# Kernel tuning notes

Hardware: AMD Instinct MI355X
Metric: run time of the kernel (lower is better)

The kernel has to match this reference:

```python
import jax, jax.numpy as jnp
import numpy as np

B, D, C, P = 1024, 768, 150, 64  # batch, in_feats, num_labels, proj2 dim
POS_M, NEG_M = 0.7, 1.4


def setup_inputs() -> dict:
    key = jax.random.key(0)
    ks = jax.random.split(key, 8)
    return {
        "x": jax.random.normal(ks[0], (B, D), jnp.float32),
        "lb": jax.random.randint(ks[1], (B,), 0, C + 1),
        "mem": jax.random.normal(ks[2], (C, D), jnp.float32),
        "fc_w": jax.random.normal(ks[3], (2 * D, 2 * D), jnp.float32) * 0.02,
        "fc_b": jnp.zeros((2 * D,), jnp.float32),
        "p1_w": jax.random.normal(ks[4], (1, 2 * D), jnp.float32) * 0.02,
        "p1_b": jnp.zeros((1,), jnp.float32),
        "p2_w": jax.random.normal(ks[5], (P, 2 * D), jnp.float32) * 0.02,
        "p2_b": jnp.zeros((P,), jnp.float32),
    }


def reference(x, lb, mem, fc_w, fc_b, p1_w, p1_b, p2_w, p2_b):
    d = x.shape[1]
    # cat([a, b], 1) @ fc_w.T == a @ Wx.T + b @ Wm.T  (exact split of the linear)
    Wx, Wm = fc_w[:, :d], fc_w[:, d:]
    xh = x @ Wx.T + fc_b                                # [B, 2D]

    # --- get_logit ---
    seen_h = jax.nn.relu(xh[:, None, :] + mem @ Wm.T)   # [B, C, 2D]
    seen = jnp.einsum('bce,e->bc', seen_h, p1_w[0]) + p1_b[0]   # [B, C]
    uh = jax.nn.relu(xh)                                # cat([x, zeros]) path
    unseen = uh @ p1_w.T + p1_b                         # [B, 1]
    logits = jnp.concatenate([seen, unseen], axis=1)    # [B, C+1]

    # --- masked log-softmax losses (pos_adapte) ---
    labels = jax.nn.one_hot(lb, C + 1, dtype=jnp.float32)
    th = jnp.zeros_like(labels).at[:, -1].set(1.0)
    labels = labels.at[:, -1].set(0.0)
    p_mask = labels + th
    n_mask = 1.0 - labels
    BIG = 1e30
    loss1 = -(jax.nn.log_softmax(logits - (1.0 - p_mask) * BIG, -1) * labels).sum(1)
    loss2 = -(jax.nn.log_softmax(logits - (1.0 - n_mask) * BIG, -1) * th).sum(1)
    loss_cls = (loss1 + loss2).mean()

    # --- metric loss on unseen embedding ---
    u = uh @ p2_w.T + p2_b                              # [B, 64]
    u = u / jnp.maximum(jnp.linalg.norm(u, axis=1, keepdims=True), 1e-12)
    sq_n = (u * u).sum(1)
    sq = sq_n[:, None] + sq_n[None, :] - 2.0 * (u @ u.T)
    err = sq <= 0.0
    dist = jnp.sqrt(jnp.clip(sq, 1e-16, None)) * (~err).astype(u.dtype)
    same = lb[:, None] == lb[None, :]
    eye = jnp.eye(dist.shape[0], dtype=bool)
    pos = (same & ~eye).astype(dist.dtype)
    neg = (~same).astype(dist.dtype)
    pos_l = (jax.nn.relu(dist - POS_M) * pos).sum() / jnp.maximum(pos.sum(), 1.0)
    neg_l = (jax.nn.relu(NEG_M - dist) * neg).sum() / jnp.maximum(neg.sum(), 1.0)

    return loss_cls + pos_l + neg_l
```

## Files before the change

kernel.cpp:

```cpp
#include <hip/hip_runtime.h>
#include <math.h>

#define B_    1024
#define D_    768
#define C_    150
#define P_    64
#define TWOD  1536
#define NCLS  151
#define CPAD  256

#define ECHUNKS 16
#define ECHUNK  96

#define GSTR  72
#define GBUF  (64 * GSTR)
#define NKT   (D_ / 64)
#define USTRU 120
#define USTR  72

#define NBLK  512

#define OFF_MH      0
#define OFF_XH      (OFF_MH + (C_ * TWOD) / 2)
#define OFF_PARTIAL (OFF_XH + (B_ * TWOD) / 2)
#define OFF_UHF     (OFF_PARTIAL + ECHUNKS * B_ * CPAD)
#define OFF_SQN     (OFF_UHF + (B_ * P_) / 2)
#define OFF_CLS     (OFF_SQN + B_)
#define OFF_PAIR    (OFF_CLS + B_)
#define OFF_BAR     (OFF_PAIR + 1024)

typedef __bf16    bfx8   __attribute__((ext_vector_type(8)));
typedef _Float16  fp16x8 __attribute__((ext_vector_type(8)));
typedef _Float16  h2v    __attribute__((ext_vector_type(2)));
typedef float     f32x4  __attribute__((ext_vector_type(4)));

__device__ inline ushort f2bf(float f) {
    union { float f; unsigned u; } c; c.f = f;
    unsigned r = c.u + 0x7fffu + ((c.u >> 16) & 1u);
    return (ushort)(r >> 16);
}
__device__ inline ushort f2h(float f) {
    _Float16 h = (_Float16)f;
    return __builtin_bit_cast(ushort, h);
}
__device__ inline uint4 pack_bf8(float4 a, float4 b) {
    uint4 r;
    r.x = (unsigned)f2bf(a.x) | ((unsigned)f2bf(a.y) << 16);
    r.y = (unsigned)f2bf(a.z) | ((unsigned)f2bf(a.w) << 16);
    r.z = (unsigned)f2bf(b.x) | ((unsigned)f2bf(b.y) << 16);
    r.w = (unsigned)f2bf(b.z) | ((unsigned)f2bf(b.w) << 16);
    return r;
}
__device__ inline uint4 pack_h8(float4 a, float4 b) {
    uint4 r;
    r.x = (unsigned)f2h(a.x) | ((unsigned)f2h(a.y) << 16);
    r.y = (unsigned)f2h(a.z) | ((unsigned)f2h(a.w) << 16);
    r.z = (unsigned)f2h(b.x) | ((unsigned)f2h(b.y) << 16);
    r.w = (unsigned)f2h(b.z) | ((unsigned)f2h(b.w) << 16);
    return r;
}
__device__ inline unsigned addrelu2(unsigned a, unsigned m) {
    h2v s = __builtin_bit_cast(h2v, a) + __builtin_bit_cast(h2v, m);
    h2v z = {(_Float16)0.f, (_Float16)0.f};
    s = __builtin_elementwise_max(s, z);
    return __builtin_bit_cast(unsigned, s);
}
__device__ inline unsigned relu2(unsigned a) {
    h2v s = __builtin_bit_cast(h2v, a);
    h2v z = {(_Float16)0.f, (_Float16)0.f};
    s = __builtin_elementwise_max(s, z);
    return __builtin_bit_cast(unsigned, s);
}
__device__ inline float dot2acc(unsigned a, unsigned b, float c) {
    return __builtin_amdgcn_fdot2(__builtin_bit_cast(h2v, a),
                                  __builtin_bit_cast(h2v, b), c, false);
}

__device__ __forceinline__ void st_wt_u16(ushort* p, unsigned v) {
    asm volatile("global_store_short %0, %1, off sc0 sc1"
                 :: "v"(p), "v"(v) : "memory");
}
__device__ __forceinline__ void st_wt_f32(float* p, float v) {
    asm volatile("global_store_dword %0, %1, off sc0 sc1"
                 :: "v"(p), "v"(v) : "memory");
}
__device__ __forceinline__ void st_wt_f32x4(float* p, f32x4 v) {
    asm volatile("global_store_dwordx4 %0, %1, off sc0 sc1"
                 :: "v"(p), "v"(v) : "memory");
}

__device__ __forceinline__ void grid_barrier(int* bar, int b)
{
    asm volatile("s_waitcnt vmcnt(0)" ::: "memory");
    __syncthreads();
    if (threadIdx.x == 0) {
        int* arr = bar + (b - 1) * 8 * 16;
        int* gen = bar + 576;
        __hip_atomic_fetch_add(&arr[(blockIdx.x & 7) * 16], 1,
                               __ATOMIC_RELAXED, __HIP_MEMORY_SCOPE_AGENT);
        if (blockIdx.x == 0) {
            for (;;) {
                int s = 0;
#pragma unroll
                for (int k = 0; k < 8; ++k)
                    s += __hip_atomic_load(&arr[k * 16], __ATOMIC_RELAXED,
                                           __HIP_MEMORY_SCOPE_AGENT);
                if (s == NBLK) break;
                __builtin_amdgcn_s_sleep(1);
            }
#pragma unroll
            for (int r = 0; r < 32; ++r)
                __hip_atomic_store(&gen[r * 16], b, __ATOMIC_RELAXED,
                                   __HIP_MEMORY_SCOPE_AGENT);
        } else {
            int* myg = &gen[(blockIdx.x & 31) * 16];
            while (__hip_atomic_load(myg, __ATOMIC_RELAXED,
                                     __HIP_MEMORY_SCOPE_AGENT) < b)
                __builtin_amdgcn_s_sleep(4);
        }
        asm volatile("" ::: "memory");
    }
    __syncthreads();
}

__device__ __forceinline__ void phase_gemm(
    int id, char* smemc,
    const float* __restrict__ x, const float* __restrict__ mem,
    const float* __restrict__ fc_w, const float* __restrict__ fc_b,
    ushort* __restrict__ xh, ushort* __restrict__ mh)
{
    if (id >= 456) return;
    ushort* As = (ushort*)smemc;
    ushort* Bs = (ushort*)(smemc + 2 * GBUF * 2);
    const int t = threadIdx.x;

    const float* A; ushort* Out; int M, m0, n0, koff; bool xblk;
    if (id < 384) {
        xblk = true;  A = x;    Out = xh; M = B_;
        m0 = (id & 15) * 64; n0 = (id >> 4) * 64; koff = 0;
    } else {
        int q = id - 384;
        xblk = false; A = mem;  Out = mh; M = C_;
        m0 = (q % 3) * 64; n0 = (q / 3) * 64; koff = D_;
    }

    const int wave = t >> 6, lane = t & 63;
    const int wm = wave * 16;
    const int fm = lane & 15, quad = lane >> 4;

    const int row_a = t >> 2, qa = (t & 3) * 16;
    const int ar = min(m0 + row_a, M - 1);
    const float* Arow = A + (size_t)ar * D_ + qa;
    const float* Brow = fc_w + (size_t)(n0 + row_a) * TWOD + koff + qa;
    const int lw = row_a * GSTR + qa;

    f32x4 acc[4];
#pragma unroll
    for (int j = 0; j < 4; ++j) {
        float bv = xblk ? fc_b[n0 + j * 16 + fm] : 0.f;
        acc[j] = (f32x4){bv, bv, bv, bv};
    }

    float4 pa0 = *(const float4*)(Arow);
    float4 pa1 = *(const float4*)(Arow + 4);
    float4 pa2 = *(const float4*)(Arow + 8);
    float4 pa3 = *(const float4*)(Arow + 12);
    float4 pb0 = *(const float4*)(Brow);
    float4 pb1 = *(const float4*)(Brow + 4);
    float4 pb2 = *(const float4*)(Brow + 8);
    float4 pb3 = *(const float4*)(Brow + 12);

    for (int kt = 0; kt < NKT; ++kt) {
        ushort* Ad = As + (kt & 1) * GBUF;
        ushort* Bd = Bs + (kt & 1) * GBUF;
        *(uint4*)&Ad[lw]     = pack_bf8(pa0, pa1);
        *(uint4*)&Ad[lw + 8] = pack_bf8(pa2, pa3);
        *(uint4*)&Bd[lw]     = pack_bf8(pb0, pb1);
        *(uint4*)&Bd[lw + 8] = pack_bf8(pb2, pb3);
        __syncthreads();
        if (kt + 1 < NKT) {
            const int k1 = (kt + 1) * 64;
            pa0 = *(const float4*)(Arow + k1);
            pa1 = *(const float4*)(Arow + k1 + 4);
            pa2 = *(const float4*)(Arow + k1 + 8);
            pa3 = *(const float4*)(Arow + k1 + 12);
            pb0 = *(const float4*)(Brow + k1);
            pb1 = *(const float4*)(Brow + k1 + 4);
            pb2 = *(const float4*)(Brow + k1 + 8);
            pb3 = *(const float4*)(Brow + k1 + 12);
        }
#pragma unroll
        for (int ks = 0; ks < 2; ++ks) {
            bfx8 af = *(const bfx8*)&Ad[(wm + fm) * GSTR + ks * 32 + quad * 8];
#pragma unroll
            for (int j = 0; j < 4; ++j) {
                bfx8 bf = *(const bfx8*)&Bd[(j * 16 + fm) * GSTR + ks * 32 + quad * 8];
                acc[j] = __builtin_amdgcn_mfma_f32_16x16x32_bf16(
                    af, bf, acc[j], 0, 0, 0);
            }
        }
    }

#pragma unroll
    for (int j = 0; j < 4; ++j)
#pragma unroll
        for (int r = 0; r < 4; ++r) {
            int row = m0 + wm + quad * 4 + r;
            int col = n0 + j * 16 + fm;
            if (row < M)
                st_wt_u16(&Out[(size_t)row * TWOD + col],
                          (unsigned)f2h(acc[j][r]));
        }
}

__device__ __forceinline__ void phase_fused(
    int id, char* smem,
    const ushort* __restrict__ xh, const ushort* __restrict__ mh,
    const float* __restrict__ p1w, const float* __restrict__ p2w,
    float* __restrict__ partial)
{
    const int t  = threadIdx.x;
    const int b0 = (id & 7) * 128;
    const int y  = (id >> 3) & 3;
    const int z  = id >> 5;
    const int e0 = z * ECHUNK;

    if (y == 3) {
        ushort* Au = (ushort*)smem;
        ushort* Wu = (ushort*)(smem + 30720);
        const int wave = t >> 6, lane = t & 63;
        const int fm = lane & 15, quad = lane >> 4;

        {
            const int row = t >> 1, kh = (t & 1) * 48;
            const ushort* src = xh + (size_t)(b0 + row) * TWOD + e0 + kh;
            uint4 v[6];
#pragma unroll
            for (int i = 0; i < 6; ++i) v[i] = *(const uint4*)&src[i * 8];
#pragma unroll
            for (int i = 0; i < 6; ++i) {
                v[i].x = relu2(v[i].x); v[i].y = relu2(v[i].y);
                v[i].z = relu2(v[i].z); v[i].w = relu2(v[i].w);
                *(uint4*)&Au[row * USTRU + kh + i * 8] = v[i];
            }
        }
        {
            const int row = t >> 2, ks = (t & 3) * 24;
            const float* pw = p2w + (size_t)row * TWOD + e0 + ks;
#pragma unroll
            for (int i = 0; i < 3; ++i) {
                float4 lo = *(const float4*)&pw[i * 8];
                float4 hi = *(const float4*)&pw[i * 8 + 4];
                *(uint4*)&Wu[row * USTRU + ks + i * 8] = pack_h8(lo, hi);
            }
        }
        __syncthreads();

        f32x4 uacc[2][4];
#pragma unroll
        for (int i = 0; i < 2; ++i)
#pragma unroll
            for (int j = 0; j < 4; ++j) uacc[i][j] = (f32x4){0.f, 0.f, 0.f, 0.f};
#pragma unroll
        for (int k0 = 0; k0 < ECHUNK; k0 += 32) {
            fp16x8 af[2], bff[4];
#pragma unroll
            for (int i = 0; i < 2; ++i)
                af[i] = *(const fp16x8*)&Au[(wave * 32 + i * 16 + fm) * USTRU + k0 + quad * 8];
#pragma unroll
            for (int j = 0; j < 4; ++j)
                bff[j] = *(const fp16x8*)&Wu[(j * 16 + fm) * USTRU + k0 + quad * 8];
#pragma unroll
            for (int i = 0; i < 2; ++i)
#pragma unroll
                for (int j = 0; j < 4; ++j)
                    uacc[i][j] = __builtin_amdgcn_mfma_f32_16x16x32_f16(
                        af[i], bff[j], uacc[i][j], 0, 0, 0);
        }
#pragma unroll
        for (int i = 0; i < 2; ++i)
#pragma unroll
            for (int j = 0; j < 4; ++j)
#pragma unroll
                for (int r = 0; r < 4; ++r) {
                    int row = b0 + wave * 32 + i * 16 + quad * 4 + r;
                    st_wt_f32(&partial[((size_t)z * B_ + row) * CPAD + 192 + j * 16 + fm],
                              uacc[i][j][r]);
                }
        return;
    }

    unsigned* xT = (unsigned*)smem;
    unsigned* mT = (unsigned*)(smem + 24576);
    unsigned* wT = (unsigned*)(smem + 36864);
    const int c0 = y * 64;
    const int tm = t & 15, tn = t >> 4;

    {
        const int row = t >> 1, ph = (t & 1) * 48;
        const ushort* src = xh + (size_t)(b0 + row) * TWOD + e0 + ph;
        uint4 v[6];
#pragma unroll
        for (int i = 0; i < 6; ++i) v[i] = *(const uint4*)&src[i * 8];
#pragma unroll
        for (int i = 0; i < 6; ++i) {
            const int ep = (t & 1) * 24 + i * 4;
            xT[(ep + 0) * 128 + row] = v[i].x;
            xT[(ep + 1) * 128 + row] = v[i].y;
            xT[(ep + 2) * 128 + row] = v[i].z;
            xT[(ep + 3) * 128 + row] = v[i].w;
        }
    }
    {
        const int col = t & 63, seg = t >> 6;
        const int gc  = c0 + col;
        uint4 v[3];
        if (gc < C_) {
            const ushort* src = mh + (size_t)gc * TWOD + e0 + seg * 24;
#pragma unroll
            for (int i = 0; i < 3; ++i) v[i] = *(const uint4*)&src[i * 8];
        } else {
#pragma unroll
            for (int i = 0; i < 3; ++i) v[i] = make_uint4(0, 0, 0, 0);
        }
#pragma unroll
        for (int i = 0; i < 3; ++i) {
            const int ep = seg * 12 + i * 4;
            mT[(ep + 0) * 64 + col] = v[i].x;
            mT[(ep + 1) * 64 + col] = v[i].y;
            mT[(ep + 2) * 64 + col] = v[i].z;
            mT[(ep + 3) * 64 + col] = v[i].w;
        }
    }
    if (t < 12) {
        float4 lo = *(const float4*)&p1w[e0 + t * 8];
        float4 hi = *(const float4*)&p1w[e0 + t * 8 + 4];
        uint4 v = pack_h8(lo, hi);
        wT[t * 4 + 0] = v.x; wT[t * 4 + 1] = v.y;
        wT[t * 4 + 2] = v.z; wT[t * 4 + 3] = v.w;
    }
    __syncthreads();

    float acc[8][4] = {};
#pragma unroll 4
    for (int ep = 0; ep < 48; ++ep) {
        uint4 a0 = *(const uint4*)&xT[ep * 128 + tm * 8];
        uint4 a1 = *(const uint4*)&xT[ep * 128 + tm * 8 + 4];
        uint4 mj = *(const uint4*)&mT[ep * 64 + tn * 4];
        const unsigned wv = wT[ep];
        const unsigned aa[8] = {a0.x, a0.y, a0.z, a0.w, a1.x, a1.y, a1.z, a1.w};
        const unsigned mm[4] = {mj.x, mj.y, mj.z, mj.w};
#pragma unroll
        for (int i = 0; i < 8; ++i)
#pragma unroll
            for (int j = 0; j < 4; ++j)
                acc[i][j] = dot2acc(addrelu2(aa[i], mm[j]), wv, acc[i][j]);
    }

#pragma unroll
    for (int i = 0; i < 8; ++i) {
        const int gb = b0 + tm * 8 + i;
        f32x4 v = {acc[i][0], acc[i][1], acc[i][2], acc[i][3]};
        st_wt_f32x4(&partial[((size_t)z * B_ + gb) * CPAD + c0 + tn * 4], v);
    }
}

__device__ __forceinline__ void phase_reduce(
    char* smemc,
    const float* __restrict__ partial,
    const float* __restrict__ p1b, const float* __restrict__ p2b,
    const int* __restrict__ lb,
    ushort* __restrict__ uhf, float* __restrict__ sqn,
    float* __restrict__ clsbuf)
{
    float* sval = (float*)smemc;
    const int t = threadIdx.x;
    for (int b = blockIdx.x; b < B_; b += NBLK) {
        float v = 0.f;
#pragma unroll
        for (int z = 0; z < ECHUNKS; ++z)
            v += partial[((size_t)z * B_ + b) * CPAD + t];
        if (t < NCLS)       v += p1b[0];
        else if (t >= 192)  v += p2b[t - 192];

        sval[t] = v;
        __syncthreads();

        if (t < 64) {
            float uv = sval[192 + t];
            float s = uv * uv;
#pragma unroll
            for (int off = 32; off; off >>= 1) s += __shfl_xor(s, off);
            float inv = 1.f / fmaxf(sqrtf(s), 1e-12f);
            st_wt_u16(&uhf[(size_t)b * P_ + t], (unsigned)f2h(uv * inv));
            if (t == 0) st_wt_f32(&sqn[b], s * inv * inv);

            const int l = lb[b];
            float mx = -1e30f;
            for (int j = t; j < NCLS; j += 64)
                if (!(j == l && l < C_)) mx = fmaxf(mx, sval[j]);
#pragma unroll
            for (int off = 32; off; off >>= 1) mx = fmaxf(mx, __shfl_xor(mx, off));
            float se = 0.f;
            for (int j = t; j < NCLS; j += 64)
                if (!(j == l && l < C_)) se += expf(sval[j] - mx);
#pragma unroll
            for (int off = 32; off; off >>= 1) se += __shfl_xor(se, off);

            if (t == 0) {
                float l150  = sval[C_];
                float loss2 = mx + logf(se) - l150;
                float loss1 = 0.f;
                if (l < C_) {
                    float a  = sval[l];
                    float m2 = fmaxf(a, l150);
                    loss1 = m2 - a + logf(expf(a - m2) + expf(l150 - m2));
                }
                st_wt_f32(&clsbuf[b], loss1 + loss2);
            }
        }
        __syncthreads();
    }
}

__device__ __forceinline__ void phase_pair(
    int id, char* smemc,
    const ushort* __restrict__ uhf, const float* __restrict__ sqn,
    const int* __restrict__ lb, float* __restrict__ pairpart)
{
    ushort* ui_s = (ushort*)smemc;
    ushort* uj_s = (ushort*)(smemc + 9216);
    float*  sni  = (float*)(smemc + 18432);
    float*  snj  = (float*)(smemc + 18688);
    int*    li   = (int*)(smemc + 18944);
    int*    lj   = (int*)(smemc + 19200);
    float*  red  = (float*)(smemc + 19456);

    const int t  = threadIdx.x;
    const int i0 = (id & 15) * 64, j0 = (id >> 4) * 64;

    for (int idx = t; idx < 512; idx += 256) {
        int row = idx >> 3, ch = (idx & 7) * 8;
        *(uint4*)&ui_s[row * USTR + ch] =
            *(const uint4*)&uhf[(size_t)(i0 + row) * P_ + ch];
        *(uint4*)&uj_s[row * USTR + ch] =
            *(const uint4*)&uhf[(size_t)(j0 + row) * P_ + ch];
    }
    if (t < 64)       { sni[t] = sqn[i0 + t]; li[t] = lb[i0 + t]; }
    else if (t < 128) { int q = t - 64; snj[q] = sqn[j0 + q]; lj[q] = lb[j0 + q]; }
    __syncthreads();

    const int wave = t >> 6, lane = t & 63;
    const int n = lane & 15, quad = lane >> 4;
    const int iw = wave * 16;

    const fp16x8 af0 = *(const fp16x8*)&ui_s[(iw + n) * USTR + quad * 8];
    const fp16x8 af1 = *(const fp16x8*)&ui_s[(iw + n) * USTR + quad * 8 + 32];

    f32x4 acc[4];
#pragma unroll
    for (int jt = 0; jt < 4; ++jt) {
        const fp16x8 bf0 = *(const fp16x8*)&uj_s[(jt * 16 + n) * USTR + quad * 8];
        const fp16x8 bf1 = *(const fp16x8*)&uj_s[(jt * 16 + n) * USTR + quad * 8 + 32];
        acc[jt] = __builtin_amdgcn_mfma_f32_16x16x32_f16(
            af0, bf0, (f32x4){0.f, 0.f, 0.f, 0.f}, 0, 0, 0);
        acc[jt] = __builtin_amdgcn_mfma_f32_16x16x32_f16(
            af1, bf1, acc[jt], 0, 0, 0);
    }

    float ps = 0.f, pc = 0.f, ns = 0.f, nc = 0.f;
#pragma unroll
    for (int jt = 0; jt < 4; ++jt)
#pragma unroll
        for (int r = 0; r < 4; ++r) {
            const int il = iw + quad * 4 + r;
            const int jl = jt * 16 + n;
            float sq = sni[il] + snj[jl] - 2.f * acc[jt][r];
            float dist = sq > 0.f ? sqrtf(fmaxf(sq, 1e-16f)) : 0.f;
            bool same = (li[il] == lj[jl]);
            if (same) {
                if (i0 + il != j0 + jl) { ps += fmaxf(dist - 0.7f, 0.f); pc += 1.f; }
            } else {
                ns += fmaxf(1.4f - dist, 0.f); nc += 1.f;
            }
        }

#pragma unroll
    for (int off = 32; off; off >>= 1) {
        ps += __shfl_xor(ps, off); pc += __shfl_xor(pc, off);
        ns += __shfl_xor(ns, off); nc += __shfl_xor(nc, off);
    }
    if (lane == 0) { red[0 * 4 + wave] = ps; red[1 * 4 + wave] = pc;
                     red[2 * 4 + wave] = ns; red[3 * 4 + wave] = nc; }
    __syncthreads();
    if (t == 0) {
        f32x4 v;
        v[0] = red[0] + red[1] + red[2] + red[3];
        v[1] = red[4] + red[5] + red[6] + red[7];
        v[2] = red[8] + red[9] + red[10] + red[11];
        v[3] = red[12] + red[13] + red[14] + red[15];
        st_wt_f32x4(&pairpart[(size_t)id * 4], v);
    }
}

__device__ __forceinline__ void phase_final(
    char* smemc,
    const float* __restrict__ clsbuf, const float* __restrict__ pairpart,
    float* __restrict__ out)
{
    float* red = (float*)smemc;
    const int t = threadIdx.x;
    float c = clsbuf[t] + clsbuf[t + 256] + clsbuf[t + 512] + clsbuf[t + 768];
    float4 pp = *(const float4*)&pairpart[(size_t)t * 4];
    float ps = pp.x, pc = pp.y, ns = pp.z, nc = pp.w;
#pragma unroll
    for (int off = 32; off; off >>= 1) {
        c  += __shfl_xor(c, off);
        ps += __shfl_xor(ps, off); pc += __shfl_xor(pc, off);
        ns += __shfl_xor(ns, off); nc += __shfl_xor(nc, off);
    }
    const int wave = t >> 6, lane = t & 63;
    if (lane == 0) { red[0 * 4 + wave] = c; red[1 * 4 + wave] = ps;
                     red[2 * 4 + wave] = pc; red[3 * 4 + wave] = ns;
                     red[4 * 4 + wave] = nc; }
    __syncthreads();
    if (t == 0) {
        float C = 0.f, PS = 0.f, PC = 0.f, NS = 0.f, NC = 0.f;
#pragma unroll
        for (int w = 0; w < 4; ++w) {
            C += red[0 * 4 + w]; PS += red[1 * 4 + w]; PC += red[2 * 4 + w];
            NS += red[3 * 4 + w]; NC += red[4 * 4 + w];
        }
        out[0] = C / (float)B_ + PS / fmaxf(PC, 1.f) + NS / fmaxf(NC, 1.f);
    }
}

__global__ __launch_bounds__(256, 2) void mega(
    const float* __restrict__ x, const int* __restrict__ lb,
    const float* __restrict__ mem, const float* __restrict__ fc_w,
    const float* __restrict__ fc_b, const float* __restrict__ p1w,
    const float* __restrict__ p1b, const float* __restrict__ p2w,
    const float* __restrict__ p2b,
    float* ws, float* out)
{
    __shared__ __align__(16) char smem[46080];

    ushort* mh       = (ushort*)(ws + OFF_MH);
    ushort* xh       = (ushort*)(ws + OFF_XH);
    float*  partial  = ws + OFF_PARTIAL;
    ushort* uhf      = (ushort*)(ws + OFF_UHF);
    float*  sqn      = ws + OFF_SQN;
    float*  clsbuf   = ws + OFF_CLS;
    float*  pairpart = ws + OFF_PAIR;
    int*    bar      = (int*)(ws + OFF_BAR);

    const int id = blockIdx.x;

    phase_gemm(id, smem, x, mem, fc_w, fc_b, xh, mh);
    grid_barrier(bar, 1);
    phase_fused(id, smem, xh, mh, p1w, p2w, partial);
    grid_barrier(bar, 2);
    phase_reduce(smem, partial, p1b, p2b, lb, uhf, sqn, clsbuf);
    grid_barrier(bar, 3);
    if (id < 256) phase_pair(id, smem, uhf, sqn, lb, pairpart);

    asm volatile("s_waitcnt vmcnt(0)" ::: "memory");
    __syncthreads();
    if (threadIdx.x == 0) {
        int* arr = bar + 3 * 8 * 16;
        __hip_atomic_fetch_add(&arr[(blockIdx.x & 7) * 16], 1,
                               __ATOMIC_RELAXED, __HIP_MEMORY_SCOPE_AGENT);
    }
    if (blockIdx.x == 0) {
        if (threadIdx.x == 0) {
            int* arr = bar + 3 * 8 * 16;
            for (;;) {
                int s = 0;
#pragma unroll
                for (int k = 0; k < 8; ++k)
                    s += __hip_atomic_load(&arr[k * 16], __ATOMIC_RELAXED,
                                           __HIP_MEMORY_SCOPE_AGENT);
                if (s == NBLK) break;
                __builtin_amdgcn_s_sleep(1);
            }
        }
        asm volatile("" ::: "memory");
        __syncthreads();
        phase_final(smem, clsbuf, pairpart, out);
    }
}

extern "C" void kernel_launch(void* const* d_in, const int* in_sizes, int n_in,
                              void* d_out, int out_size, void* d_ws, size_t ws_size,
                              hipStream_t stream)
{
    const float* x    = (const float*)d_in[0];
    const int*   lb   = (const int*)d_in[1];
    const float* mem  = (const float*)d_in[2];
    const float* fc_w = (const float*)d_in[3];
    const float* fc_b = (const float*)d_in[4];
    const float* p1w  = (const float*)d_in[5];
    const float* p1b  = (const float*)d_in[6];
    const float* p2w  = (const float*)d_in[7];
    const float* p2b  = (const float*)d_in[8];

    float* ws  = (float*)d_ws;
    int*   bar = (int*)(ws + OFF_BAR);

    hipMemsetAsync(bar, 0, 8192, stream);

    mega<<<NBLK, 256, 0, stream>>>(x, lb, mem, fc_w, fc_b,
                                   p1w, p1b, p2w, p2b, ws, (float*)d_out);
}
```

Before: 132.7 us.

## Use persistent generation-counted grid barrier and pad transposed LDS tile

Measured after the change: 131.5 us. No clear change (-0.9%).

```diff
diff --git a/kernel.cpp b/kernel.cpp
--- a/kernel.cpp
+++ b/kernel.cpp
@@ -17,6 +17,7 @@
 #define NKT   (D_ / 64)
 #define USTRU 120
 #define USTR  72
+#define XSTR  192
 
 #define NBLK  512
 
@@ -27,12 +28,14 @@
 #define OFF_SQN     (OFF_UHF + (B_ * P_) / 2)
 #define OFF_CLS     (OFF_SQN + B_)
 #define OFF_PAIR    (OFF_CLS + B_)
-#define OFF_BAR     (OFF_PAIR + 1024)
 
 typedef __bf16    bfx8   __attribute__((ext_vector_type(8)));
 typedef _Float16  fp16x8 __attribute__((ext_vector_type(8)));
 typedef _Float16  h2v    __attribute__((ext_vector_type(2)));
 typedef float     f32x4  __attribute__((ext_vector_type(4)));
+
+__device__ int g_arr[8 * 16];
+__device__ int g_gen[32 * 16];
 
 __device__ inline ushort f2bf(float f) {
     union { float f; unsigned u; } c; c.f = f;
@@ -89,33 +92,33 @@
                  :: "v"(p), "v"(v) : "memory");
 }
 
-__device__ __forceinline__ void grid_barrier(int* bar, int b)
+__device__ __forceinline__ void grid_barrier(int G0, int b)
 {
     asm volatile("s_waitcnt vmcnt(0)" ::: "memory");
     __syncthreads();
     if (threadIdx.x == 0) {
-        int* arr = bar + (b - 1) * 8 * 16;
-        int* gen = bar + 576;
-        __hip_atomic_fetch_add(&arr[(blockIdx.x & 7) * 16], 1,
+        const int target = G0 + b;
+        __hip_atomic_fetch_add(&g_arr[(blockIdx.x & 7) * 16], 1,
                                __ATOMIC_RELAXED, __HIP_MEMORY_SCOPE_AGENT);
         if (blockIdx.x == 0) {
+            const int starget = NBLK * target;
             for (;;) {
                 int s = 0;
 #pragma unroll
                 for (int k = 0; k < 8; ++k)
-                    s += __hip_atomic_load(&arr[k * 16], __ATOMIC_RELAXED,
+                    s += __hip_atomic_load(&g_arr[k * 16], __ATOMIC_RELAXED,
                                            __HIP_MEMORY_SCOPE_AGENT);
-                if (s == NBLK) break;
+                if (s - starget >= 0) break;
                 __builtin_amdgcn_s_sleep(1);
             }
 #pragma unroll
             for (int r = 0; r < 32; ++r)
-                __hip_atomic_store(&gen[r * 16], b, __ATOMIC_RELAXED,
+                __hip_atomic_store(&g_gen[r * 16], target, __ATOMIC_RELAXED,
                                    __HIP_MEMORY_SCOPE_AGENT);
         } else {
-            int* myg = &gen[(blockIdx.x & 31) * 16];
+            int* myg = &g_gen[(blockIdx.x & 31) * 16];
             while (__hip_atomic_load(myg, __ATOMIC_RELAXED,
-                                     __HIP_MEMORY_SCOPE_AGENT) < b)
+                                     __HIP_MEMORY_SCOPE_AGENT) - target < 0)
                 __builtin_amdgcn_s_sleep(4);
         }
         asm volatile("" ::: "memory");
@@ -291,13 +294,14 @@
     }
 
     unsigned* xT = (unsigned*)smem;
-    unsigned* mT = (unsigned*)(smem + 24576);
-    unsigned* wT = (unsigned*)(smem + 36864);
+    unsigned* mT = (unsigned*)(smem + 36864);
+    unsigned* wT = (unsigned*)(smem + 49152);
     const int c0 = y * 64;
     const int tm = t & 15, tn = t >> 4;
 
     {
         const int row = t >> 1, ph = (t & 1) * 48;
+        const int rowo = row + ((row >> 3) << 2);
         const ushort* src = xh + (size_t)(b0 + row) * TWOD + e0 + ph;
         uint4 v[6];
 #pragma unroll
@@ -305,10 +309,10 @@
 #pragma unroll
         for (int i = 0; i < 6; ++i) {
             const int ep = (t & 1) * 24 + i * 4;
-            xT[(ep + 0) * 128 + row] = v[i].x;
-            xT[(ep + 1) * 128 + row] = v[i].y;
-            xT[(ep + 2) * 128 + row] = v[i].z;
-            xT[(ep + 3) * 128 + row] = v[i].w;
+            xT[(ep + 0) * XSTR + rowo] = v[i].x;
+            xT[(ep + 1) * XSTR + rowo] = v[i].y;
+            xT[(ep + 2) * XSTR + rowo] = v[i].z;
+            xT[(ep + 3) * XSTR + rowo] = v[i].w;
         }
     }
     {
@@ -344,8 +348,8 @@
     float acc[8][4] = {};
 #pragma unroll 4
     for (int ep = 0; ep < 48; ++ep) {
-        uint4 a0 = *(const uint4*)&xT[ep * 128 + tm * 8];
-        uint4 a1 = *(const uint4*)&xT[ep * 128 + tm * 8 + 4];
+        uint4 a0 = *(const uint4*)&xT[ep * XSTR + tm * 12];
+        uint4 a1 = *(const uint4*)&xT[ep * XSTR + tm * 12 + 4];
         uint4 mj = *(const uint4*)&mT[ep * 64 + tn * 4];
         const unsigned wv = wT[ep];
         const unsigned aa[8] = {a0.x, a0.y, a0.z, a0.w, a1.x, a1.y, a1.z, a1.w};
@@ -543,7 +547,7 @@
     const float* __restrict__ p2b,
     float* ws, float* out)
 {
-    __shared__ __align__(16) char smem[46080];
+    __shared__ __align__(16) char smem[49344];
 
     ushort* mh       = (ushort*)(ws + OFF_MH);
     ushort* xh       = (ushort*)(ws + OFF_XH);
@@ -552,37 +556,46 @@
     float*  sqn      = ws + OFF_SQN;
     float*  clsbuf   = ws + OFF_CLS;
     float*  pairpart = ws + OFF_PAIR;
-    int*    bar      = (int*)(ws + OFF_BAR);
 
     const int id = blockIdx.x;
 
+    int G0 = 0;
+    if (threadIdx.x == 0) {
+        G0 = __hip_atomic_load(&g_gen[(blockIdx.x & 31) * 16],
+                               __ATOMIC_RELAXED, __HIP_MEMORY_SCOPE_AGENT);
+        asm volatile("s_waitcnt vmcnt(0)" ::: "memory");
+    }
+
     phase_gemm(id, smem, x, mem, fc_w, fc_b, xh, mh);
-    grid_barrier(bar, 1);
+    grid_barrier(G0, 1);
     phase_fused(id, smem, xh, mh, p1w, p2w, partial);
-    grid_barrier(bar, 2);
+    grid_barrier(G0, 2);
     phase_reduce(smem, partial, p1b, p2b, lb, uhf, sqn, clsbuf);
-    grid_barrier(bar, 3);
+    grid_barrier(G0, 3);
     if (id < 256) phase_pair(id, smem, uhf, sqn, lb, pairpart);
 
     asm volatile("s_waitcnt vmcnt(0)" ::: "memory");
     __syncthreads();
     if (threadIdx.x == 0) {
-        int* arr = bar + 3 * 8 * 16;
-        __hip_atomic_fetch_add(&arr[(blockIdx.x & 7) * 16], 1,
+        __hip_atomic_fetch_add(&g_arr[(blockIdx.x & 7) * 16], 1,
                                __ATOMIC_RELAXED, __HIP_MEMORY_SCOPE_AGENT);
     }
     if (blockIdx.x == 0) {
         if (threadIdx.x == 0) {
-            int* arr = bar + 3 * 8 * 16;
+            const int starget = NBLK * (G0 + 4);
             for (;;) {
                 int s = 0;
 #pragma unroll
                 for (int k = 0; k < 8; ++k)
-                    s += __hip_atomic_load(&arr[k * 16], __ATOMIC_RELAXED,
+                    s += __hip_atomic_load(&g_arr[k * 16], __ATOMIC_RELAXED,
                                            __HIP_MEMORY_SCOPE_AGENT);
-                if (s == NBLK) break;
+                if (s - starget >= 0) break;
                 __builtin_amdgcn_s_sleep(1);
             }
+#pragma unroll
+            for (int r = 0; r < 32; ++r)
+                __hip_atomic_store(&g_gen[r * 16], G0 + 4, __ATOMIC_RELAXED,
+                                   __HIP_MEMORY_SCOPE_AGENT);
         }
         asm volatile("" ::: "memory");
         __syncthreads();
@@ -604,10 +617,7 @@
     const float* p2w  = (const float*)d_in[7];
     const float* p2b  = (const float*)d_in[8];
 
-    float* ws  = (float*)d_ws;
-    int*   bar = (int*)(ws + OFF_BAR);
-
-    hipMemsetAsync(bar, 0, 8192, stream);
+    float* ws = (float*)d_ws;
 
     mega<<<NBLK, 256, 0, stream>>>(x, lb, mem, fc_w, fc_b,
                                    p1w, p1b, p2w, p2b, ws, (float*)d_out);
```
